# Kernel tuning notes

Hardware: AMD Instinct MI355X
Metric: run time of the kernel (lower is better)

## Reference

```python
import jax, jax.numpy as jnp
import numpy as np

N_NODES = 50000
N_EDGES = 800000
N_GRAPHS = 2048
NODE_F = 30
EDGE_F = 8
HID = 32
HEADS = 4
NEG_SLOPE = 0.2


def _gat_conv(x, src, dst, eattr, W, a_src, a_dst, We, a_edge, b):
    # x: [N, Fin]; src/dst: [E'] (self-loops already appended); eattr: [E', edge_dim]
    N = x.shape[0]
    H, C = a_src.shape
    h = (x @ W).reshape(N, H, C)                     # [N,H,C]
    e = (eattr @ We).reshape(-1, H, C)               # [E',H,C]
    al_s = jnp.sum(h * a_src, axis=-1)               # [N,H]
    al_d = jnp.sum(h * a_dst, axis=-1)               # [N,H]
    al_e = jnp.sum(e * a_edge, axis=-1)              # [E',H]
    alpha = al_s[src] + al_d[dst] + al_e             # [E',H]
    alpha = jax.nn.leaky_relu(alpha, NEG_SLOPE)
    # segment softmax over destination nodes (every node has a self-loop)
    mx = jax.ops.segment_max(alpha, dst, num_segments=N)
    alpha = jnp.exp(alpha - mx[dst])
    den = jax.ops.segment_sum(alpha, dst, num_segments=N)
    alpha = alpha / (den[dst] + 1e-16)
    msg = h[src] * alpha[:, :, None]                 # [E',H,C]
    out = jax.ops.segment_sum(msg, dst, num_segments=N)  # [N,H,C]
    return out.reshape(N, H * C) + b


def _make_params(key):
    ks = jax.random.split(key, 32)
    i = 0
    p = {}
    def nxt(shape, scale=0.1):
        nonlocal i
        k = ks[i]; i += 1
        return jax.random.normal(k, shape, dtype=jnp.float32) * scale
    dims = [(NODE_F, HEADS * HID), (HEADS * HID, HEADS * HID), (HEADS * HID, HEADS * HID)]
    for li, (fin, fout) in enumerate(dims, 1):
        p[f"W{li}"] = nxt((fin, fout))
        p[f"att_src{li}"] = nxt((HEADS, HID))
        p[f"att_dst{li}"] = nxt((HEADS, HID))
        p[f"We{li}"] = nxt((EDGE_F, HEADS * HID))
        p[f"att_e{li}"] = nxt((HEADS, HID))
        p[f"b{li}"] = nxt((HEADS * HID,))
    p["lw1"] = nxt((HEADS * HID, HID)); p["lb1"] = nxt((HID,))
    p["lw2"] = nxt((HID, HID)); p["lb2"] = nxt((HID,))
    p["lw3"] = nxt((HID, 1)); p["lb3"] = nxt((1,))
    return p


def setup_inputs() -> dict:
    key = jax.random.key(0)
    k1, k2, k3, k4, k5 = jax.random.split(key, 5)
    x = jax.random.normal(k1, (N_NODES, NODE_F), dtype=jnp.float32)
    edge_index = jax.random.randint(k2, (2, N_EDGES), 0, N_NODES, dtype=jnp.int64)
    edge_features = jax.random.normal(k3, (N_EDGES, EDGE_F), dtype=jnp.float32)
    batch = jnp.sort(jax.random.randint(k4, (N_NODES,), 0, N_GRAPHS, dtype=jnp.int64))
    inp = {"x": x, "edge_index": edge_index, "edge_features": edge_features, "batch": batch}
    inp.update(_make_params(k5))
    return inp


def reference(x, edge_index, edge_features, batch,
              W1, att_src1, att_dst1, We1, att_e1, b1,
              W2, att_src2, att_dst2, We2, att_e2, b2,
              W3, att_src3, att_dst3, We3, att_e3, b3,
              lw1, lb1, lw2, lb2, lw3, lb3):
    N = x.shape[0]
    # add self-loops (PyG GATConv default); self-loop edge_attr = mean of edge_attr
    loop = jnp.arange(N, dtype=edge_index.dtype)
    src = jnp.concatenate([edge_index[0], loop])
    dst = jnp.concatenate([edge_index[1], loop])
    mean_e = jnp.mean(edge_features, axis=0, keepdims=True)
    eattr = jnp.concatenate([edge_features, jnp.broadcast_to(mean_e, (N, EDGE_F))], axis=0)

    h = jax.nn.relu(_gat_conv(x, src, dst, eattr, W1, att_src1, att_dst1, We1, att_e1, b1))
    h = jax.nn.relu(_gat_conv(h, src, dst, eattr, W2, att_src2, att_dst2, We2, att_e2, b2))
    h = jax.nn.relu(_gat_conv(h, src, dst, eattr, W3, att_src3, att_dst3, We3, att_e3, b3))
    # global_add_pool
    g = jax.ops.segment_sum(h, batch, num_segments=N_GRAPHS)   # [G, H*C]
    g = jax.nn.relu(g @ lw1 + lb1)
    g = jax.nn.relu(g @ lw2 + lb2)
    g = jax.nn.relu(g @ lw3 + lb3)                              # [G, 1]
    return g
```

## Files before the change

### kernel.cpp

```cpp
#include <hip/hip_runtime.h>
#include <hip/hip_fp16.h>

#define NND 50000
#define NE  800000
#define NG  2048
#define MB  1024
#define CAP 56

typedef __attribute__((ext_vector_type(8))) short short8;
typedef __attribute__((ext_vector_type(4))) float float4v;

__device__ __forceinline__ float frelu(float v){ return v > 0.f ? v : 0.f; }

__device__ __forceinline__ unsigned short f2bf(float f){
    unsigned int u = __float_as_uint(f);
    u += 0x7FFFu + ((u >> 16) & 1u);
    return (unsigned short)(u >> 16);
}
__device__ __forceinline__ float bf2f(unsigned short s){
    return __uint_as_float(((unsigned int)s) << 16);
}

__global__ __launch_bounds__(256) void k_mean(const float4* __restrict__ ef4,
                                              float* __restrict__ partial,
                                              float* __restrict__ gz,
                                              int* __restrict__ cntz,
                                              int* __restrict__ srcarr){
    __shared__ float4 red[256];
    int t = threadIdx.x;
    int i0 = blockIdx.x * 256 + t;
    gz[i0] = 0.f;
    if (i0 < NND){
        cntz[i0] = 0;
        srcarr[i0 * CAP] = i0;
    }
    const int S = MB * 256;
    float4 a = make_float4(0.f, 0.f, 0.f, 0.f);
    for (int j = i0; j < NE * 2; j += S){
        float4 v = ef4[j];
        a.x += v.x; a.y += v.y; a.z += v.z; a.w += v.w;
    }
    red[t] = a;
    __syncthreads();
    for (int off = 128; off >= 2; off >>= 1){
        if (t < off){
            float4 o = red[t + off];
            float4 m = red[t];
            m.x += o.x; m.y += o.y; m.z += o.z; m.w += o.w;
            red[t] = m;
        }
        __syncthreads();
    }
    if (t < 8){
        float v = (t < 4) ? ((const float*)&red[0])[t]
                          : ((const float*)&red[1])[t - 4];
        partial[blockIdx.x * 8 + t] = v;
    }
}

__global__ void k_prep(const float* __restrict__ partial,
                       const float* __restrict__ We1, const float* __restrict__ ae1,
                       const float* __restrict__ We2, const float* __restrict__ ae2,
                       const float* __restrict__ We3, const float* __restrict__ ae3,
                       float* __restrict__ M, float* __restrict__ sc){
    __shared__ float me[8];
    __shared__ float pm[16][8];
    __shared__ float Ms[96];
    int t = threadIdx.x;
    {
        int ch = t & 7, seg = t >> 3;
        float s = 0.f;
        for (int j = seg; j < MB; j += 16) s += partial[j * 8 + ch];
        pm[seg][ch] = s;
    }
    __syncthreads();
    if (t < 8){
        float s = 0.f;
        for (int i = 0; i < 16; i++) s += pm[i][t];
        me[t] = s * (1.0f / NE);
    }
    if (t < 96){
        int l = t >> 5, f = (t >> 2) & 7, h = t & 3;
        const float* We = (l == 0) ? We1 : ((l == 1) ? We2 : We3);
        const float* ae = (l == 0) ? ae1 : ((l == 1) ? ae2 : ae3);
        float s = 0.f;
        for (int c = 0; c < 32; c++) s += We[f * 128 + h * 32 + c] * ae[h * 32 + c];
        M[t] = s; Ms[t] = s;
    }
    __syncthreads();
    if (t < 12){
        int l = t >> 2, h = t & 3;
        float s = 0.f;
        for (int f = 0; f < 8; f++) s += me[f] * Ms[l * 32 + f * 4 + h];
        sc[t] = s;
    }
}

template<int FIN, int FINR, int BFIN>
__global__ __launch_bounds__(256) void k_gemm(
        const void* __restrict__ xv, const float* __restrict__ W,
        const float* __restrict__ asrc, const float* __restrict__ adst,
        unsigned short* __restrict__ h, float* __restrict__ als,
        float* __restrict__ ald){
    constexpr int KS = FIN + 8;
    constexpr int SZ1 = 64 * KS + 128 * KS;
    constexpr int SZ2 = 64 * 136;
    constexpr int LSZ = SZ1 > SZ2 ? SZ1 : SZ2;
    __shared__ unsigned short lds[LSZ];
    unsigned short* xa = lds;
    unsigned short* wb = lds + 64 * KS;
    int t = threadIdx.x;
    int r0 = blockIdx.x * 64;

    if (BFIN){
        const unsigned int* xu = (const unsigned int*)xv;
        for (int i = t; i < 64 * (FIN / 2); i += 256){
            int r = i / (FIN / 2), kp = i % (FIN / 2);
            int gr = r0 + r;
            unsigned int pk = (gr < NND) ? xu[gr * (FINR / 2) + kp] : 0u;
            *(unsigned int*)&xa[r * KS + 2 * kp] = pk;
        }
    } else {
        const float* x = (const float*)xv;
        for (int i = t; i < 64 * (FIN / 2); i += 256){
            int r = i / (FIN / 2), kp = i % (FIN / 2);
            int gr = r0 + r, k = 2 * kp;
            float v0 = 0.f, v1 = 0.f;
            if (gr < NND){
                if (k     < FINR) v0 = x[gr * FINR + k];
                if (k + 1 < FINR) v1 = x[gr * FINR + k + 1];
            }
            unsigned int pk = (unsigned int)f2bf(v0) | ((unsigned int)f2bf(v1) << 16);
            *(unsigned int*)&xa[r * KS + k] = pk;
        }
    }
    for (int i = t; i < 128 * (FIN / 2); i += 256){
        int n = i & 127, kp = i >> 7, k = 2 * kp;
        float v0 = (k     < FINR) ? W[k * 128 + n]       : 0.f;
        float v1 = (k + 1 < FINR) ? W[(k + 1) * 128 + n] : 0.f;
        unsigned int pk = (unsigned int)f2bf(v0) | ((unsigned int)f2bf(v1) << 16);
        *(unsigned int*)&wb[n * KS + k] = pk;
    }
    __syncthreads();

    int wv = t >> 6, lane = t & 63;
    int quad = lane >> 4, lrow = lane & 15;
    int arow = wv * 16 + lrow;
    int koff = quad * 8;
    float4v acc[8];
    #pragma unroll
    for (int nt = 0; nt < 8; nt++) acc[nt] = (float4v){0.f, 0.f, 0.f, 0.f};
    #pragma unroll
    for (int ks = 0; ks < FIN / 32; ks++){
        short8 af = *(const short8*)&xa[arow * KS + ks * 32 + koff];
        #pragma unroll
        for (int nt = 0; nt < 8; nt++){
            short8 bf = *(const short8*)&wb[(nt * 16 + lrow) * KS + ks * 32 + koff];
            acc[nt] = __builtin_amdgcn_mfma_f32_16x16x32_bf16(af, bf, acc[nt], 0, 0, 0);
        }
    }
    __syncthreads();
    unsigned short* hb = lds;
    #pragma unroll
    for (int nt = 0; nt < 8; nt++){
        #pragma unroll
        for (int reg = 0; reg < 4; reg++){
            int lr = wv * 16 + quad * 4 + reg;
            hb[lr * 136 + nt * 16 + lrow] = f2bf(acc[nt][reg]);
        }
    }
    __syncthreads();
    {
        int r = t >> 2, hd = t & 3;
        int gr = r0 + r;
        float sa = 0.f, sd = 0.f;
        const unsigned short* hp = &hb[r * 136 + hd * 32];
        #pragma unroll
        for (int c = 0; c < 32; c++){
            float hv = bf2f(hp[c]);
            sa += hv * asrc[hd * 32 + c];
            sd += hv * adst[hd * 32 + c];
        }
        if (gr < NND){ als[gr * 4 + hd] = sa; ald[gr * 4 + hd] = sd; }
    }
    for (int i = t; i < 64 * 16; i += 256){
        int r = i >> 4, c8 = i & 15;
        int gr = r0 + r;
        if (gr < NND)
            *(int4*)&h[gr * 128 + c8 * 8] = *(const int4*)&hb[r * 136 + c8 * 8];
    }
}

__global__ void k_hist(const int* __restrict__ ei, int* __restrict__ cnt,
                       int* __restrict__ pose, int* __restrict__ srcarr){
    int e = blockIdx.x * 256 + threadIdx.x;
    if (e >= NE) return;
    int s = ei[e];
    int d = ei[NE + e];
    int pos = atomicAdd(&cnt[d], 1);
    pose[e] = pos;
    srcarr[d * CAP + 1 + pos] = s;
}

__global__ __launch_bounds__(256) void k_weight(
        const int* __restrict__ ei, const float* __restrict__ ef,
        const float4* __restrict__ als4, const float4* __restrict__ ald4,
        const float* __restrict__ Mg, const float* __restrict__ sc4g,
        const int* __restrict__ pose, uint2* __restrict__ wS){
    __shared__ float Ms[32];
    __shared__ float Scs[4];
    int t = threadIdx.x;
    if (t < 32) Ms[t] = Mg[t];
    if (t < 4)  Scs[t] = sc4g[t];
    __syncthreads();
    int e = blockIdx.x * 256 + t;
    if (e < NE){
        int s = ei[e], d = ei[NE + e];
        const float4* efp = (const float4*)ef;
        float4 u = efp[e * 2], v = efp[e * 2 + 1];
        float4 A = als4[s], D = ald4[d];
        float wp[4];
        const float* Ap = &A.x; const float* Dp = &D.x;
        #pragma unroll
        for (int h = 0; h < 4; h++){
            float ae = u.x * Ms[0 + h]  + u.y * Ms[4 + h]
                     + u.z * Ms[8 + h]  + u.w * Ms[12 + h]
                     + v.x * Ms[16 + h] + v.y * Ms[20 + h]
                     + v.z * Ms[24 + h] + v.w * Ms[28 + h];
            float a = Ap[h] + Dp[h] + ae;
            a = a > 0.f ? a : 0.2f * a;
            wp[h] = __expf(a);
        }
        __half2 a01 = __floats2half2_rn(wp[0], wp[1]);
        __half2 a23 = __floats2half2_rn(wp[2], wp[3]);
        uint2 pk = make_uint2(*(unsigned int*)&a01, *(unsigned int*)&a23);
        wS[ei[NE + e] * CAP + 1 + pose[e]] = pk;
    } else if (e < NE + NND){
        int n = e - NE;
        float4 A = als4[n], D = ald4[n];
        float wp[4];
        const float* Ap = &A.x; const float* Dp = &D.x;
        #pragma unroll
        for (int h = 0; h < 4; h++){
            float a = Ap[h] + Dp[h] + Scs[h];
            a = a > 0.f ? a : 0.2f * a;
            wp[h] = __expf(a);
        }
        __half2 a01 = __floats2half2_rn(wp[0], wp[1]);
        __half2 a23 = __floats2half2_rn(wp[2], wp[3]);
        wS[n * CAP] = make_uint2(*(unsigned int*)&a01, *(unsigned int*)&a23);
    }
}

__global__ __launch_bounds__(256) void k_gather(
        const int* __restrict__ srcarr, const int* __restrict__ cntA,
        const __half* __restrict__ wH,
        const unsigned int* __restrict__ HU,
        const float* __restrict__ b, unsigned int* __restrict__ outU){
    int wid  = threadIdx.x >> 6;
    int lane = threadIdx.x & 63;
    int n = blockIdx.x * 4 + wid;
    int start = n * CAP;
    int cnt = cntA[n] + 1;
    int mh = lane >> 4;
    float ax = 0.f, ay = 0.f, accw = 0.f;

    int s[8]; float w[8];
    int k = 0;
    if (cnt >= 8){
        #pragma unroll
        for (int j = 0; j < 8; j++){
            int i = start + j;
            s[j] = srcarr[i];
            w[j] = __half2float(wH[i * 4 + mh]);
        }
    }
    while (k + 8 <= cnt){
        int cs[8]; float cw[8];
        #pragma unroll
        for (int j = 0; j < 8; j++){ cs[j] = s[j]; cw[j] = w[j]; }
        k += 8;
        if (k + 8 <= cnt){
            #pragma unroll
            for (int j = 0; j < 8; j++){
                int i = start + k + j;
                s[j] = srcarr[i];
                w[j] = __half2float(wH[i * 4 + mh]);
            }
        }
        unsigned int hv[8];
        #pragma unroll
        for (int j = 0; j < 8; j++) hv[j] = HU[cs[j] * 64 + lane];
        #pragma unroll
        for (int j = 0; j < 8; j++){
            float lo = __uint_as_float(hv[j] << 16);
            float hi = __uint_as_float(hv[j] & 0xFFFF0000u);
            ax += cw[j] * lo;
            ay += cw[j] * hi;
            accw += cw[j];
        }
    }
    int rem = cnt - k;
    if (rem > 0){
        int ts[8]; float tw[8];
        #pragma unroll
        for (int j = 0; j < 8; j++){
            bool v = j < rem;
            int i = v ? (start + k + j) : start;
            ts[j] = srcarr[i];
            tw[j] = v ? __half2float(wH[i * 4 + mh]) : 0.f;
        }
        unsigned int hv[8];
        #pragma unroll
        for (int j = 0; j < 8; j++) hv[j] = HU[ts[j] * 64 + lane];
        #pragma unroll
        for (int j = 0; j < 8; j++){
            float lo = __uint_as_float(hv[j] << 16);
            float hi = __uint_as_float(hv[j] & 0xFFFF0000u);
            ax += tw[j] * lo;
            ay += tw[j] * hi;
            accw += tw[j];
        }
    }
    float inv = 1.f / (accw + 1e-16f);
    int c0 = 2 * lane;
    float ox = frelu(ax * inv + b[c0]);
    float oy = frelu(ay * inv + b[c0 + 1]);
    outU[n * 64 + lane] = (unsigned int)f2bf(ox) | ((unsigned int)f2bf(oy) << 16);
}

__global__ __launch_bounds__(128) void k_pool(const unsigned short* __restrict__ y,
                                              const int* __restrict__ batch,
                                              float* __restrict__ g){
    int c = threadIdx.x;
    int n0 = blockIdx.x * 32;
    if (n0 >= NND) return;
    int cur = batch[n0];
    float s = 0.f;
    for (int k = 0; k < 32; k++){
        int n = n0 + k;
        if (n >= NND) break;
        int bg = batch[n];
        if (bg != cur){
            atomicAdd(&g[cur * 128 + c], s);
            s = 0.f; cur = bg;
        }
        s += bf2f(y[n * 128 + c]);
    }
    atomicAdd(&g[cur * 128 + c], s);
}

__global__ void k_mlp(const float* __restrict__ g,
                      const float* __restrict__ lw1, const float* __restrict__ lb1,
                      const float* __restrict__ lw2, const float* __restrict__ lb2,
                      const float* __restrict__ lw3, const float* __restrict__ lb3,
                      float* __restrict__ out){
    __shared__ float t1[4][32];
    __shared__ float t2[4][32];
    int tid = threadIdx.x, sub = tid >> 5, j = tid & 31;
    int gi = blockIdx.x * 4 + sub;
    const float* gr = g + gi * 128;
    float s = lb1[j];
    for (int c = 0; c < 128; c++) s += gr[c] * lw1[c * 32 + j];
    t1[sub][j] = frelu(s);
    __syncthreads();
    float s2 = lb2[j];
    for (int k = 0; k < 32; k++) s2 += t1[sub][k] * lw2[k * 32 + j];
    t2[sub][j] = frelu(s2);
    __syncthreads();
    if (j == 0){
        float o = lb3[0];
        for (int k = 0; k < 32; k++) o += t2[sub][k] * lw3[k];
        out[gi] = frelu(o);
    }
}

extern "C" void kernel_launch(void* const* d_in, const int* in_sizes, int n_in,
                              void* d_out, int out_size, void* d_ws, size_t ws_size,
                              hipStream_t stream) {
    const float* x     = (const float*)d_in[0];
    const int*   ei    = (const int*)  d_in[1];
    const float* ef    = (const float*)d_in[2];
    const int*   batch = (const int*)  d_in[3];
    const float* W[3]   = {(const float*)d_in[4],  (const float*)d_in[10], (const float*)d_in[16]};
    const float* as_[3] = {(const float*)d_in[5],  (const float*)d_in[11], (const float*)d_in[17]};
    const float* ad_[3] = {(const float*)d_in[6],  (const float*)d_in[12], (const float*)d_in[18]};
    const float* We[3]  = {(const float*)d_in[7],  (const float*)d_in[13], (const float*)d_in[19]};
    const float* ae[3]  = {(const float*)d_in[8],  (const float*)d_in[14], (const float*)d_in[20]};
    const float* b_[3]  = {(const float*)d_in[9],  (const float*)d_in[15], (const float*)d_in[21]};
    const float* lw1 = (const float*)d_in[22]; const float* lb1 = (const float*)d_in[23];
    const float* lw2 = (const float*)d_in[24]; const float* lb2 = (const float*)d_in[25];
    const float* lw3 = (const float*)d_in[26]; const float* lb3 = (const float*)d_in[27];

    float* ws = (float*)d_ws;
    float* Bx   = ws;
    float* Hbf  = Bx + 3200000;
    float* wSf  = Hbf + 3200000;
    float* als  = wSf + 5600000;
    float* ald  = als + 200000;
    float* g    = ald + 200000;
    float* partial = g + 262144;
    float* M    = partial + MB * 8;
    float* sc   = M + 96;
    int*   srcarr = (int*)(sc + 16);
    int*   pose   = srcarr + NND * CAP;
    int*   cnt    = pose + NE;

    unsigned short* Hb = (unsigned short*)Hbf;

    k_mean<<<MB, 256, 0, stream>>>((const float4*)ef, partial, g, cnt, srcarr);
    k_prep<<<1, 128, 0, stream>>>(partial, We[0], ae[0], We[1], ae[1], We[2], ae[2], M, sc);
    k_hist<<<(NE + 255) / 256, 256, 0, stream>>>(ei, cnt, pose, srcarr);

    const int GB = (NND + 63) / 64;
    for (int l = 0; l < 3; l++){
        if (l == 0)
            k_gemm<32, 30, 0><<<GB, 256, 0, stream>>>(x, W[l], as_[l], ad_[l],
                                                      Hb, als, ald);
        else
            k_gemm<128, 128, 1><<<GB, 256, 0, stream>>>(Bx, W[l], as_[l], ad_[l],
                                                        Hb, als, ald);
        k_weight<<<(NE + NND + 255) / 256, 256, 0, stream>>>(
            ei, ef, (const float4*)als, (const float4*)ald,
            M + l * 32, sc + l * 4, pose, (uint2*)wSf);
        k_gather<<<NND / 4, 256, 0, stream>>>(srcarr, cnt, (const __half*)wSf,
                                              (const unsigned int*)Hb, b_[l],
                                              (unsigned int*)Bx);
    }

    k_pool<<<(NND + 31) / 32, 128, 0, stream>>>((const unsigned short*)Bx, batch, g);
    k_mlp<<<NG / 4, 128, 0, stream>>>(g, lw1, lb1, lw2, lb2, lw3, lb3, (float*)d_out);
}
```

Measured before the change: 476.8 us.

## Pack source index and attention weights into one 16-byte CSR record

Replaces the separate per-slot source-index array and half-precision weight array with a single uint4 record per CSR slot holding the source id and four fp16 head weights. The weight kernel now writes the source id alongside the weights every layer, k_hist only counts positions, and the gather kernel loads one 16-byte record per neighbor instead of two scattered loads. This trades an extra source-id write and 4 bytes of padding per slot in each layer for fewer load instructions and cache lines touched in the gather.

```diff
diff --git a/kernel.cpp b/kernel.cpp
--- a/kernel.cpp
+++ b/kernel.cpp
@@ -20,20 +20,20 @@
 __device__ __forceinline__ float bf2f(unsigned short s){
     return __uint_as_float(((unsigned int)s) << 16);
 }
+__device__ __forceinline__ float h2f(unsigned short bits){
+    __half hv = __ushort_as_half(bits);
+    return __half2float(hv);
+}
 
 __global__ __launch_bounds__(256) void k_mean(const float4* __restrict__ ef4,
                                               float* __restrict__ partial,
                                               float* __restrict__ gz,
-                                              int* __restrict__ cntz,
-                                              int* __restrict__ srcarr){
+                                              int* __restrict__ cntz){
     __shared__ float4 red[256];
     int t = threadIdx.x;
     int i0 = blockIdx.x * 256 + t;
     gz[i0] = 0.f;
-    if (i0 < NND){
-        cntz[i0] = 0;
-        srcarr[i0 * CAP] = i0;
-    }
+    if (i0 < NND) cntz[i0] = 0;
     const int S = MB * 256;
     float4 a = make_float4(0.f, 0.f, 0.f, 0.f);
     for (int j = i0; j < NE * 2; j += S){
@@ -192,21 +192,18 @@
 }
 
 __global__ void k_hist(const int* __restrict__ ei, int* __restrict__ cnt,
-                       int* __restrict__ pose, int* __restrict__ srcarr){
+                       int* __restrict__ pose){
     int e = blockIdx.x * 256 + threadIdx.x;
     if (e >= NE) return;
-    int s = ei[e];
     int d = ei[NE + e];
-    int pos = atomicAdd(&cnt[d], 1);
-    pose[e] = pos;
-    srcarr[d * CAP + 1 + pos] = s;
+    pose[e] = atomicAdd(&cnt[d], 1);
 }
 
 __global__ __launch_bounds__(256) void k_weight(
         const int* __restrict__ ei, const float* __restrict__ ef,
         const float4* __restrict__ als4, const float4* __restrict__ ald4,
         const float* __restrict__ Mg, const float* __restrict__ sc4g,
-        const int* __restrict__ pose, uint2* __restrict__ wS){
+        const int* __restrict__ pose, uint4* __restrict__ rec){
     __shared__ float Ms[32];
     __shared__ float Scs[4];
     int t = threadIdx.x;
@@ -233,8 +230,8 @@
         }
         __half2 a01 = __floats2half2_rn(wp[0], wp[1]);
         __half2 a23 = __floats2half2_rn(wp[2], wp[3]);
-        uint2 pk = make_uint2(*(unsigned int*)&a01, *(unsigned int*)&a23);
-        wS[ei[NE + e] * CAP + 1 + pose[e]] = pk;
+        rec[d * CAP + 1 + pose[e]] =
+            make_uint4((unsigned int)s, *(unsigned int*)&a01, *(unsigned int*)&a23, 0u);
     } else if (e < NE + NND){
         int n = e - NE;
         float4 A = als4[n], D = ald4[n];
@@ -248,13 +245,13 @@
         }
         __half2 a01 = __floats2half2_rn(wp[0], wp[1]);
         __half2 a23 = __floats2half2_rn(wp[2], wp[3]);
-        wS[n * CAP] = make_uint2(*(unsigned int*)&a01, *(unsigned int*)&a23);
+        rec[n * CAP] =
+            make_uint4((unsigned int)n, *(unsigned int*)&a01, *(unsigned int*)&a23, 0u);
     }
 }
 
 __global__ __launch_bounds__(256) void k_gather(
-        const int* __restrict__ srcarr, const int* __restrict__ cntA,
-        const __half* __restrict__ wH,
+        const uint4* __restrict__ rec, const int* __restrict__ cntA,
         const unsigned int* __restrict__ HU,
         const float* __restrict__ b, unsigned int* __restrict__ outU){
     int wid  = threadIdx.x >> 6;
@@ -263,6 +260,8 @@
     int start = n * CAP;
     int cnt = cntA[n] + 1;
     int mh = lane >> 4;
+    int word  = mh >> 1;
+    int shift = (mh & 1) * 16;
     float ax = 0.f, ay = 0.f, accw = 0.f;
 
     int s[8]; float w[8];
@@ -270,9 +269,10 @@
     if (cnt >= 8){
         #pragma unroll
         for (int j = 0; j < 8; j++){
-            int i = start + j;
-            s[j] = srcarr[i];
-            w[j] = __half2float(wH[i * 4 + mh]);
+            uint4 r = rec[start + j];
+            s[j] = (int)r.x;
+            unsigned int wb = word ? r.z : r.y;
+            w[j] = h2f((unsigned short)(wb >> shift));
         }
     }
     while (k + 8 <= cnt){
@@ -283,9 +283,10 @@
         if (k + 8 <= cnt){
             #pragma unroll
             for (int j = 0; j < 8; j++){
-                int i = start + k + j;
-                s[j] = srcarr[i];
-                w[j] = __half2float(wH[i * 4 + mh]);
+                uint4 r = rec[start + k + j];
+                s[j] = (int)r.x;
+                unsigned int wb = word ? r.z : r.y;
+                w[j] = h2f((unsigned short)(wb >> shift));
             }
         }
         unsigned int hv[8];
@@ -307,8 +308,11 @@
         for (int j = 0; j < 8; j++){
             bool v = j < rem;
             int i = v ? (start + k + j) : start;
-            ts[j] = srcarr[i];
-            tw[j] = v ? __half2float(wH[i * 4 + mh]) : 0.f;
+            uint4 r = rec[i];
+            ts[j] = (int)r.x;
+            unsigned int wb = word ? r.z : r.y;
+            float wj = h2f((unsigned short)(wb >> shift));
+            tw[j] = v ? wj : 0.f;
         }
         unsigned int hv[8];
         #pragma unroll
@@ -395,22 +399,21 @@
     float* ws = (float*)d_ws;
     float* Bx   = ws;
     float* Hbf  = Bx + 3200000;
-    float* wSf  = Hbf + 3200000;
-    float* als  = wSf + 5600000;
+    float* als  = Hbf + 3200000;
     float* ald  = als + 200000;
     float* g    = ald + 200000;
     float* partial = g + 262144;
     float* M    = partial + MB * 8;
     float* sc   = M + 96;
-    int*   srcarr = (int*)(sc + 16);
-    int*   pose   = srcarr + NND * CAP;
-    int*   cnt    = pose + NE;
+    uint4* rec  = (uint4*)(sc + 16);
+    int*   pose = (int*)(rec + NND * CAP);
+    int*   cnt  = pose + NE;
 
     unsigned short* Hb = (unsigned short*)Hbf;
 
-    k_mean<<<MB, 256, 0, stream>>>((const float4*)ef, partial, g, cnt, srcarr);
+    k_mean<<<MB, 256, 0, stream>>>((const float4*)ef, partial, g, cnt);
     k_prep<<<1, 128, 0, stream>>>(partial, We[0], ae[0], We[1], ae[1], We[2], ae[2], M, sc);
-    k_hist<<<(NE + 255) / 256, 256, 0, stream>>>(ei, cnt, pose, srcarr);
+    k_hist<<<(NE + 255) / 256, 256, 0, stream>>>(ei, cnt, pose);
 
     const int GB = (NND + 63) / 64;
     for (int l = 0; l < 3; l++){
@@ -422,8 +425,8 @@
                                                         Hb, als, ald);
         k_weight<<<(NE + NND + 255) / 256, 256, 0, stream>>>(
             ei, ef, (const float4*)als, (const float4*)ald,
-            M + l * 32, sc + l * 4, pose, (uint2*)wSf);
-        k_gather<<<NND / 4, 256, 0, stream>>>(srcarr, cnt, (const __half*)wSf,
+            M + l * 32, sc + l * 4, pose, rec);
+        k_gather<<<NND / 4, 256, 0, stream>>>(rec, cnt,
                                               (const unsigned int*)Hb, b_[l],
                                               (unsigned int*)Bx);
     }
```

After: 481.5 us. No clear change (+1.0%).
